# Performance work log

Measured on AMD Instinct MI355X. Metric: run time of the kernel, lower is better.

Reference implementation:

```python
import jax, jax.numpy as jnp
import numpy as np

LORA_RANK = 16
LORA_ALPHA = 32
CHUNK_SIZE = 64
TTT_LR = 0.01
SCALING = LORA_ALPHA / LORA_RANK  # 2.0

B, S = 2, 2048
K_DIM, H_DIM = 11008, 4096
EMBED_DIM, VOCAB = 4096, 32000


def setup_inputs() -> dict:
    key = jax.random.key(0)
    ks = jax.random.split(key, 7)
    x = jax.random.normal(ks[0], (B, S, K_DIM), jnp.float32) * 0.02
    input_ids = jax.random.randint(ks[1], (B, S), 0, VOCAB)
    W_base = jax.random.normal(ks[2], (H_DIM, K_DIM), jnp.float32) * 0.02
    embed_table = jax.random.normal(ks[3], (VOCAB, EMBED_DIM), jnp.float32) * 0.02
    W_proj = jax.random.normal(ks[4], (H_DIM, EMBED_DIM), jnp.float32) * 0.02
    init_A = jax.random.normal(ks[5], (H_DIM, LORA_RANK), jnp.float32) * 0.02
    init_B = jax.random.normal(ks[6], (LORA_RANK, K_DIM), jnp.float32) * 0.02
    return dict(x=x, W_base=W_base, embed_table=embed_table, W_proj=W_proj,
                init_A=init_A, init_B=init_B, input_ids=input_ids)


def reference(x, W_base, embed_table, W_proj, init_A, init_B, input_ids):
    # base (frozen) linear: x [B,S,k] @ W_base^T [k,h]
    base_out = jnp.einsum('bsk,hk->bsh', x, W_base)

    # TTT targets: embedding of NEXT token (shift-by-1, zero-padded), frozen lookup
    embeds = embed_table[input_ids]  # [B,S,E]
    shifted = jnp.concatenate([embeds[:, 1:, :], jnp.zeros_like(embeds[:, :1, :])], axis=1)
    V = jnp.einsum('bse,he->bsh', shifted, W_proj)  # [B,S,h]

    Bsz, Seq, k = x.shape
    h = W_base.shape[0]
    pad = (-Seq) % CHUNK_SIZE
    Zp = jnp.pad(x, ((0, 0), (0, pad), (0, 0)))
    Vp = jnp.pad(V, ((0, 0), (0, pad), (0, 0)))
    nc = Zp.shape[1] // CHUNK_SIZE
    Z = Zp.reshape(Bsz, nc, CHUNK_SIZE, k)    # [B,N,C,k]
    Vc = Vp.reshape(Bsz, nc, CHUNK_SIZE, h)   # [B,N,C,h]

    # per-chunk fast updates
    # dA = V^T @ (Z @ B^T) : [B,N,h,r]
    proj_in = jnp.einsum('bnck,rk->bncr', Z, init_B)
    dA = jnp.einsum('bnch,bncr->bnhr', Vc, proj_in)
    # dB = (V @ A)^T @ Z : [B,N,r,k]
    proj_err = jnp.einsum('bnch,hr->bncr', Vc, init_A)
    dB = jnp.einsum('bncr,bnck->bnrk', proj_err, Z)

    # exclusive prefix-sum over chunks (chunk i sees updates from chunks < i)
    csA = jnp.cumsum(dA, axis=1)
    csB = jnp.cumsum(dB, axis=1)
    accA = jnp.concatenate([jnp.zeros_like(csA[:, :1]), csA[:, :-1]], axis=1)
    accB = jnp.concatenate([jnp.zeros_like(csB[:, :1]), csB[:, :-1]], axis=1)

    lr = TTT_LR * SCALING
    A_eff = init_A[None, None] - lr * accA  # [B,N,h,r]
    B_eff = init_B[None, None] - lr * accB  # [B,N,r,k]

    mid = jnp.einsum('bnck,bnrk->bncr', Z, B_eff)
    lora = jnp.einsum('bncr,bnhr->bnch', mid, A_eff)  # [B,N,C,h]
    lora = lora.reshape(Bsz, nc * CHUNK_SIZE, h)[:, :Seq]
    return base_out + lora * SCALING
```

## Files before the change

kernel.cpp:

```cpp
#include <hip/hip_runtime.h>

typedef __attribute__((ext_vector_type(8))) short bf16x8;
typedef __attribute__((ext_vector_type(4))) float f32x4;

__device__ __forceinline__ float b2f(short s) {
  return __uint_as_float(((unsigned int)(unsigned short)s) << 16);
}
__device__ __forceinline__ short f2b(float f) {
  unsigned int u = __float_as_uint(f);
  unsigned int r = (u + 0x7fffu + ((u >> 16) & 1u)) >> 16;
  return (short)(unsigned short)r;
}

#define GLOAD16(g, l) __builtin_amdgcn_global_load_lds( \
    (const __attribute__((address_space(1))) void*)(g),  \
    (__attribute__((address_space(3))) void*)(l), 16, 0, 0)

__global__ __launch_bounds__(256) void prep1(const float* __restrict__ x,
    const float* __restrict__ wb, const float* __restrict__ wp,
    short* __restrict__ dst) {
  const long NX = 5636096L, NW = 11272192L, NT = 13369344L;
  for (long it = (long)blockIdx.x * 256 + threadIdx.x; it < NT;
       it += (long)gridDim.x * 256) {
    const float* s; long off;
    if (it < NX)      { s = x;  off = it; }
    else if (it < NW) { s = wb; off = it - NX; }
    else              { s = wp; off = it - NW; }
    float4 a = *(const float4*)(s + off * 8);
    float4 b = *(const float4*)(s + off * 8 + 4);
    bf16x8 o;
    o[0] = f2b(a.x); o[1] = f2b(a.y); o[2] = f2b(a.z); o[3] = f2b(a.w);
    o[4] = f2b(b.x); o[5] = f2b(b.y); o[6] = f2b(b.z); o[7] = f2b(b.w);
    *(bf16x8*)(dst + it * 8) = o;
  }
}

__global__ __launch_bounds__(256) void prep2(const float* __restrict__ initB,
    short* __restrict__ iBb, const float* __restrict__ initA,
    short* __restrict__ iAt, const float* __restrict__ emb,
    const int* __restrict__ ids, short* __restrict__ shb) {
  const long N1 = 22016L, N2 = 26112L, NT = 2123264L;
  for (long it = (long)blockIdx.x * 256 + threadIdx.x; it < NT;
       it += (long)gridDim.x * 256) {
    if (it < N1) {
      float4 a = *(const float4*)(initB + it * 8);
      float4 b = *(const float4*)(initB + it * 8 + 4);
      bf16x8 o;
      o[0] = f2b(a.x); o[1] = f2b(a.y); o[2] = f2b(a.z); o[3] = f2b(a.w);
      o[4] = f2b(b.x); o[5] = f2b(b.y); o[6] = f2b(b.z); o[7] = f2b(b.w);
      *(bf16x8*)(iBb + it * 8) = o;
    } else if (it < N2) {
      const int h = (int)(it - N1);
      #pragma unroll
      for (int r = 0; r < 16; ++r)
        iAt[(long)r * 4096 + h] = f2b(initA[(long)h * 16 + r]);
    } else {
      const long i3 = it - N2;
      const int token = (int)(i3 >> 9);
      const int e = ((int)i3 & 511) * 8;
      const int s = token & 2047;
      const int row = (s == 2047) ? -1 : ids[token + 1];
      bf16x8 o;
      if (row < 0) {
        #pragma unroll
        for (int j = 0; j < 8; ++j) o[j] = 0;
      } else {
        float4 a = *(const float4*)(emb + (long)row * 4096 + e);
        float4 b = *(const float4*)(emb + (long)row * 4096 + e + 4);
        o[0] = f2b(a.x); o[1] = f2b(a.y); o[2] = f2b(a.z); o[3] = f2b(a.w);
        o[4] = f2b(b.x); o[5] = f2b(b.y); o[6] = f2b(b.z); o[7] = f2b(b.w);
      }
      *(bf16x8*)(shb + (long)token * 4096 + e) = o;
    }
  }
}

template <int OUTBF16>
__global__ __launch_bounds__(512, 2) void gemm8p(const short* __restrict__ A,
    const short* __restrict__ B, void* __restrict__ C, int M, int N, int Kd) {
  __shared__ short lds[65536];
  const int tid = threadIdx.x;
  const int lane = tid & 63;
  const int wid = tid >> 6;
  const int wr = wid >> 2;
  const int wcn = wid & 3;
  const int l15 = lane & 15, l4 = lane >> 4, l7 = lane & 7;
  const int lb = (lane >> 3) & 1;

  const int nbx = N >> 8;
  const int cpx = gridDim.x >> 3;
  const int wg = ((int)blockIdx.x & 7) * cpx + ((int)blockIdx.x >> 3);
  const long m0 = (long)(wg / nbx) * 256;
  const long n0 = (long)(wg % nbx) * 256;

  const int NT = Kd >> 6;

  const int rho = lane >> 3;
  const short* Ag = A + (m0 + wid * 8 + rho) * (long)Kd + (l7 ^ rho) * 8;
  const short* Bg = B + (n0 + wid * 8 + rho) * (long)Kd + (l7 ^ rho) * 8;

#define STAGE_A(b, kt, c) GLOAD16(Ag + (long)(c) * 64 * Kd + (long)(kt) * 64, \
    (char*)lds + (b) * 65536 + ((c) * 8 + wid) * 1024 + lane * 16)
#define STAGE_B(b, kt, c) GLOAD16(Bg + (long)(c) * 64 * Kd + (long)(kt) * 64, \
    (char*)lds + (b) * 65536 + 32768 + ((c) * 8 + wid) * 1024 + lane * 16)

  int aLane[2];
  #pragma unroll
  for (int h = 0; h < 2; ++h)
    aLane[h] = (lb * 64 + l7 * 8 + ((h * 4 + l4) ^ l7)) * 16;

#define READ_A(dst, buf, c)                                                   \
  do {                                                                        \
    _Pragma("unroll")                                                         \
    for (int sub = 0; sub < 2; ++sub) {                                       \
      dst[sub][0] = *(const bf16x8*)((buf) + (c) * 8192 + wr * 4096 +         \
                                     sub * 2048 + aLane[0]);                  \
      dst[sub][1] = *(const bf16x8*)((buf) + (c) * 8192 + wr * 4096 +         \
                                     sub * 2048 + aLane[1]);                  \
    }                                                                         \
  } while (0)

#define READ_B(buf)                                                           \
  do {                                                                        \
    _Pragma("unroll")                                                         \
    for (int nf = 0; nf < 4; ++nf) {                                          \
      bv[nf][0] = *(const bf16x8*)((buf) + 32768 + wcn * 8192 + nf * 2048 +   \
                                   aLane[0]);                                 \
      bv[nf][1] = *(const bf16x8*)((buf) + 32768 + wcn * 8192 + nf * 2048 +   \
                                   aLane[1]);                                 \
    }                                                                         \
  } while (0)

#define MFMA_BLOCK(q, av)                                                     \
  do {                                                                        \
    _Pragma("unroll")                                                         \
    for (int sub = 0; sub < 2; ++sub)                                         \
      _Pragma("unroll")                                                       \
      for (int nf = 0; nf < 4; ++nf) {                                        \
        acc[(q) * 2 + sub][nf] = __builtin_amdgcn_mfma_f32_16x16x32_bf16(     \
            av[sub][0], bv[nf][0], acc[(q) * 2 + sub][nf], 0, 0, 0);          \
        acc[(q) * 2 + sub][nf] = __builtin_amdgcn_mfma_f32_16x16x32_bf16(     \
            av[sub][1], bv[nf][1], acc[(q) * 2 + sub][nf], 0, 0, 0);          \
      }                                                                       \
  } while (0)

  f32x4 acc[8][4];
  #pragma unroll
  for (int m = 0; m < 8; ++m)
    #pragma unroll
    for (int n = 0; n < 4; ++n) {
      acc[m][n][0] = 0.f; acc[m][n][1] = 0.f;
      acc[m][n][2] = 0.f; acc[m][n][3] = 0.f;
    }

  STAGE_A(0, 0, 0); STAGE_B(0, 0, 0);
  STAGE_A(0, 0, 1); STAGE_B(0, 0, 1);
  STAGE_A(0, 0, 2); STAGE_B(0, 0, 2);
  STAGE_A(0, 0, 3); STAGE_B(0, 0, 3);
  STAGE_A(1, 1, 0); STAGE_B(1, 1, 0);
  STAGE_A(1, 1, 1); STAGE_B(1, 1, 1);
  STAGE_A(1, 1, 2); STAGE_B(1, 1, 2);
  asm volatile("s_waitcnt vmcnt(6)" ::: "memory");
  __builtin_amdgcn_s_barrier();
  asm volatile("" ::: "memory");

  const char* ldsb = (const char*)lds;
  bf16x8 avX[2][2], avY[2][2], bv[4][2];
  READ_B(ldsb);
  READ_A(avX, ldsb, 0);

  for (int t = 0; t < NT; ++t) {
    const int cur = t & 1;
    const int tn1 = (t + 1 < NT) ? t + 1 : 0;
    const int tn2 = (t + 2 < NT) ? t + 2 : 0;
    const char* pc = ldsb + cur * 65536;
    const char* pn = ldsb + (cur ^ 1) * 65536;

    READ_A(avY, pc, 1);
    STAGE_A(cur ^ 1, tn1, 3); STAGE_B(cur ^ 1, tn1, 3);
    __builtin_amdgcn_s_barrier();
    asm volatile("s_waitcnt lgkmcnt(4)" ::: "memory");
    __builtin_amdgcn_sched_barrier(0);
    __builtin_amdgcn_s_setprio(1);
    MFMA_BLOCK(0, avX);
    __builtin_amdgcn_s_setprio(0);
    __builtin_amdgcn_s_barrier();
    asm volatile("" ::: "memory");

    READ_A(avX, pc, 2);
    STAGE_A(cur, tn2, 0); STAGE_B(cur, tn2, 0);
    __builtin_amdgcn_s_barrier();
    asm volatile("s_waitcnt lgkmcnt(4)" ::: "memory");
    __builtin_amdgcn_sched_barrier(0);
    __builtin_amdgcn_s_setprio(1);
    MFMA_BLOCK(1, avY);
    __builtin_amdgcn_s_setprio(0);
    __builtin_amdgcn_s_barrier();
    asm volatile("" ::: "memory");

    READ_A(avY, pc, 3);
    STAGE_A(cur, tn2, 1); STAGE_B(cur, tn2, 1);
    __builtin_amdgcn_s_barrier();
    asm volatile("s_waitcnt lgkmcnt(4)" ::: "memory");
    __builtin_amdgcn_sched_barrier(0);
    __builtin_amdgcn_s_setprio(1);
    MFMA_BLOCK(2, avX);
    __builtin_amdgcn_s_setprio(0);
    __builtin_amdgcn_s_barrier();
    asm volatile("" ::: "memory");

    STAGE_A(cur, tn2, 2); STAGE_B(cur, tn2, 2);
    asm volatile("s_waitcnt vmcnt(6)" ::: "memory");
    __builtin_amdgcn_s_barrier();
    asm volatile("s_waitcnt lgkmcnt(0)" ::: "memory");
    __builtin_amdgcn_sched_barrier(0);
    __builtin_amdgcn_s_setprio(1);
    MFMA_BLOCK(3, avY);
    __builtin_amdgcn_s_setprio(0);
    __builtin_amdgcn_sched_barrier(0);
    READ_B(pn);
    READ_A(avX, pn, 0);
    __builtin_amdgcn_s_barrier();
    asm volatile("" ::: "memory");
  }
#undef STAGE_A
#undef STAGE_B
#undef READ_A
#undef READ_B
#undef MFMA_BLOCK

  #pragma unroll
  for (int q = 0; q < 4; ++q)
    #pragma unroll
    for (int sub = 0; sub < 2; ++sub)
      #pragma unroll
      for (int nf = 0; nf < 4; ++nf)
        #pragma unroll
        for (int j = 0; j < 4; ++j) {
          const long row = m0 + q * 64 + wr * 32 + sub * 16 + l4 * 4 + j;
          const long col = n0 + wcn * 64 + nf * 16 + l15;
          if (OUTBF16) ((short*)C)[row * N + col] = f2b(acc[q * 2 + sub][nf][j]);
          else         ((float*)C)[row * N + col] = acc[q * 2 + sub][nf][j];
        }
}

__device__ __forceinline__ void gemv_core(short* lds, const short* __restrict__ A,
    const short* __restrict__ W, float* __restrict__ part, int Kd, int Klen,
    long wStride) {
  const int tid = threadIdx.x;
  const int lane = tid & 63;
  const int w = tid >> 6;
  const int l15 = lane & 15, l4 = lane >> 4;
  const int rho = lane >> 3, j7 = lane & 7;
  const long m0 = (long)blockIdx.x * 64;
  const long k0 = (long)blockIdx.y * Klen;
  const int NTk = Klen >> 6;
  const short* Wr = W + (wStride ? (long)blockIdx.x * wStride : 0);
  const short* Ag = A + (m0 + w * 8 + rho) * (long)Kd + k0 + (j7 ^ rho) * 8;

#define STG(b, kt, i) GLOAD16(Ag + (long)(i) * 32 * Kd + (long)(kt) * 64, \
    (char*)lds + (b) * 8192 + ((i) * 4 + w) * 1024 + lane * 16)

  int aOff[2];
  #pragma unroll
  for (int kk = 0; kk < 2; ++kk)
    aOff[kk] = ((w * 16 + l15) >> 3) * 1024 + (l15 & 7) * 128 +
               (((kk * 4 + l4) ^ (l15 & 7)) * 16);

  f32x4 acc; acc[0] = 0.f; acc[1] = 0.f; acc[2] = 0.f; acc[3] = 0.f;

  STG(0, 0, 0); STG(0, 0, 1);
  for (int t = 0; t < NTk; ++t) {
    const int cur = t & 1;
    const int tn = (t + 1 < NTk) ? t + 1 : 0;
    const short* wp = Wr + (long)l15 * Kd + k0 + (long)t * 64 + l4 * 8;
    bf16x8 wv0 = *(const bf16x8*)(wp);
    bf16x8 wv1 = *(const bf16x8*)(wp + 32);
    STG(cur ^ 1, tn, 0); STG(cur ^ 1, tn, 1);
    asm volatile("s_waitcnt vmcnt(2)" ::: "memory");
    __builtin_amdgcn_s_barrier();
    bf16x8 a0 = *(const bf16x8*)((const char*)lds + cur * 8192 + aOff[0]);
    bf16x8 a1 = *(const bf16x8*)((const char*)lds + cur * 8192 + aOff[1]);
    asm volatile("s_waitcnt lgkmcnt(0)" ::: "memory");
    __builtin_amdgcn_sched_barrier(0);
    acc = __builtin_amdgcn_mfma_f32_16x16x32_bf16(a0, wv0, acc, 0, 0, 0);
    acc = __builtin_amdgcn_mfma_f32_16x16x32_bf16(a1, wv1, acc, 0, 0, 0);
    __builtin_amdgcn_s_barrier();
  }
#undef STG

  float* dst = part + (long)blockIdx.y * 65536;
  #pragma unroll
  for (int r = 0; r < 4; ++r)
    dst[(m0 + w * 16 + l4 * 4 + r) * 16 + l15] = acc[r];
}

__global__ __launch_bounds__(256) void gemv_pinper(const short* __restrict__ xb,
    const short* __restrict__ iBb, float* __restrict__ pinP,
    const short* __restrict__ Vb, const short* __restrict__ iAt,
    float* __restrict__ perP) {
  __shared__ short lds[8192];
  if (blockIdx.z == 0) gemv_core(lds, xb, iBb, pinP, 11008, 2752, 0L);
  else                 gemv_core(lds, Vb, iAt, perP, 4096, 1024, 0L);
}

__global__ __launch_bounds__(256) void gemv_mid(const short* __restrict__ xb,
    const short* __restrict__ Beff, float* __restrict__ midP) {
  __shared__ short lds[8192];
  gemv_core(lds, xb, Beff, midP, 11008, 2752, 176128L);
}

__global__ __launch_bounds__(256) void dAdB_kernel(const short* __restrict__ V,
    const short* __restrict__ X, const float* __restrict__ pinP,
    const float* __restrict__ perP, float* __restrict__ dA,
    float* __restrict__ dB) {
  const int chunk = blockIdx.y;
  __shared__ float ps[1024];
  if (blockIdx.x < 16) {
    const int h = blockIdx.x * 256 + threadIdx.x;
    #pragma unroll
    for (int i = 0; i < 4; ++i) {
      const long o = (long)chunk * 1024 + i * 256 + threadIdx.x;
      ps[i * 256 + threadIdx.x] = pinP[o] + pinP[o + 65536] +
                                  pinP[o + 131072] + pinP[o + 196608];
    }
    __syncthreads();
    float acc[16];
    #pragma unroll
    for (int r = 0; r < 16; ++r) acc[r] = 0.f;
    for (int c = 0; c < 64; ++c) {
      const float v = b2f(V[((long)chunk * 64 + c) * 4096 + h]);
      #pragma unroll
      for (int r = 0; r < 16; ++r) acc[r] = fmaf(v, ps[c * 16 + r], acc[r]);
    }
    float* dst = dA + ((long)chunk * 4096 + h) * 16;
    #pragma unroll
    for (int i = 0; i < 4; ++i) {
      f32x4 w; w[0] = acc[i*4]; w[1] = acc[i*4+1]; w[2] = acc[i*4+2]; w[3] = acc[i*4+3];
      *(f32x4*)(dst + i * 4) = w;
    }
  } else {
    const int k = (blockIdx.x - 16) * 256 + threadIdx.x;
    #pragma unroll
    for (int i = 0; i < 4; ++i) {
      const long o = (long)chunk * 1024 + i * 256 + threadIdx.x;
      ps[i * 256 + threadIdx.x] = perP[o] + perP[o + 65536] +
                                  perP[o + 131072] + perP[o + 196608];
    }
    __syncthreads();
    float acc[16];
    #pragma unroll
    for (int r = 0; r < 16; ++r) acc[r] = 0.f;
    for (int c = 0; c < 64; ++c) {
      const float xv = b2f(X[((long)chunk * 64 + c) * 11008 + k]);
      #pragma unroll
      for (int r = 0; r < 16; ++r) acc[r] = fmaf(xv, ps[c * 16 + r], acc[r]);
    }
    #pragma unroll
    for (int r = 0; r < 16; ++r)
      dB[((long)chunk * 16 + r) * 11008 + k] = acc[r];
  }
}

__global__ __launch_bounds__(256) void scan_kernel(const float* __restrict__ dA,
    const float* __restrict__ initA, short* __restrict__ Aeff,
    const float* __restrict__ dB, const float* __restrict__ initB,
    short* __restrict__ Beff) {
  const int b = blockIdx.y;
  if (blockIdx.x < 256) {
    const long idx = (long)blockIdx.x * 256 + threadIdx.x;
    const float a0 = initA[idx];
    float acc = 0.f;
    for (int n = 0; n < 32; ++n) {
      const long chunk = (long)b * 32 + n;
      Aeff[chunk * 65536 + idx] = f2b(a0 - 0.02f * acc);
      acc += dA[chunk * 65536 + idx];
    }
  } else {
    const long idx = (long)(blockIdx.x - 256) * 256 + threadIdx.x;
    const float b0 = initB[idx];
    float acc = 0.f;
    for (int n = 0; n < 32; ++n) {
      const long chunk = (long)b * 32 + n;
      Beff[chunk * 176128 + idx] = f2b(b0 - 0.02f * acc);
      acc += dB[chunk * 176128 + idx];
    }
  }
}

__global__ __launch_bounds__(256) void final_kernel(const short* __restrict__ base,
    const float* __restrict__ midP, const short* __restrict__ Aeff,
    float* __restrict__ out) {
  const int token = blockIdx.x;
  const int chunk = token >> 6;
  __shared__ float m[16];
  if (threadIdx.x < 16) {
    const long o = (long)token * 16 + threadIdx.x;
    m[threadIdx.x] = midP[o] + midP[o + 65536] + midP[o + 131072] + midP[o + 196608];
  }
  __syncthreads();
  float mf[16];
  #pragma unroll
  for (int r = 0; r < 16; ++r) mf[r] = m[r];
  for (int it = 0; it < 2; ++it) {
    const int h0 = it * 2048 + threadIdx.x * 8;
    bf16x8 bs = *(const bf16x8*)(base + (long)token * 4096 + h0);
    float res[8];
    #pragma unroll
    for (int j = 0; j < 8; ++j) {
      const short* ar = Aeff + ((long)chunk * 4096 + h0 + j) * 16;
      bf16x8 a0 = *(const bf16x8*)ar;
      bf16x8 a1 = *(const bf16x8*)(ar + 8);
      float s = 0.f;
      #pragma unroll
      for (int r = 0; r < 8; ++r) {
        s = fmaf(mf[r], b2f(a0[r]), s);
        s = fmaf(mf[r + 8], b2f(a1[r]), s);
      }
      res[j] = b2f(bs[j]) + 2.0f * s;
    }
    #pragma unroll
    for (int i = 0; i < 2; ++i) {
      f32x4 w; w[0] = res[i*4]; w[1] = res[i*4+1]; w[2] = res[i*4+2]; w[3] = res[i*4+3];
      *(f32x4*)(out + (long)token * 4096 + h0 + i * 4) = w;
    }
  }
}

extern "C" void kernel_launch(void* const* d_in, const int* in_sizes, int n_in,
                              void* d_out, int out_size, void* d_ws, size_t ws_size,
                              hipStream_t stream) {
  const float* x     = (const float*)d_in[0];
  const float* Wbase = (const float*)d_in[1];
  const float* emb   = (const float*)d_in[2];
  const float* Wproj = (const float*)d_in[3];
  const float* initA = (const float*)d_in[4];
  const float* initB = (const float*)d_in[5];
  const int*   ids   = (const int*)d_in[6];
  float* outp = (float*)d_out;

  char* p = (char*)d_ws;
  short* xb   = (short*)p; p += 90177536L;
  short* Wb   = (short*)p; p += 90177536L;
  short* Wpb  = (short*)p; p += 33554432L;
  short* shb  = (short*)p; p += 33554432L;
  short* Vb   = (short*)p; p += 33554432L;
  short* base = (short*)p; p += 33554432L;
  short* iBb  = (short*)p; p += 352256L;
  short* iAt  = (short*)p; p += 131072L;
  short* Aeff = (short*)p; p += 8388608L;
  short* Beff = (short*)p; p += 22544384L;
  float* pinP = (float*)p; p += 1048576L;
  float* perP = (float*)p; p += 1048576L;
  float* midP = (float*)p; p += 1048576L;
  float* dA = (float*)Wpb;
  float* dB = (float*)((char*)Wpb + 16777216L);

  prep1<<<2048, 256, 0, stream>>>(x, Wbase, Wproj, xb);
  prep2<<<2048, 256, 0, stream>>>(initB, iBb, initA, iAt, emb, ids, shb);

  gemm8p<1><<<256, 512, 0, stream>>>(shb, Wpb, (void*)Vb, 4096, 4096, 4096);
  gemm8p<1><<<256, 512, 0, stream>>>(xb, Wb, (void*)base, 4096, 4096, 11008);

  gemv_pinper<<<dim3(64, 4, 2), 256, 0, stream>>>(xb, iBb, pinP, Vb, iAt, perP);
  dAdB_kernel<<<dim3(59, 64), 256, 0, stream>>>(Vb, xb, pinP, perP, dA, dB);
  scan_kernel<<<dim3(944, 2), 256, 0, stream>>>(dA, initA, Aeff, dB, initB, Beff);

  gemv_mid<<<dim3(64, 4), 256, 0, stream>>>(xb, Beff, midP);
  final_kernel<<<4096, 256, 0, stream>>>(base, midP, Aeff, outp);
}
```

Before: 732.0 us.

## Fuse LoRA epilogue into base GEMM and drop final kernel

The base GEMM moves to the end of the pipeline and gains an epilogue. It reduces the midP partials into LDS, computes the rank-16 LoRA correction from Aeff, and writes fp32 output directly. This removes the bf16 base intermediate (its write and later read) and the separate final kernel launch. The GEMM epilogue gets heavier and can no longer overlap with the scan and gemv stages, and the base result now stays in fp32 rather than being rounded to bf16.

```diff
diff --git a/kernel.cpp b/kernel.cpp
--- a/kernel.cpp
+++ b/kernel.cpp
@@ -75,9 +75,11 @@
   }
 }
 
-template <int OUTBF16>
+template <int FUSE>
 __global__ __launch_bounds__(512, 2) void gemm8p(const short* __restrict__ A,
-    const short* __restrict__ B, void* __restrict__ C, int M, int N, int Kd) {
+    const short* __restrict__ B, void* __restrict__ C,
+    const float* __restrict__ midP, const short* __restrict__ Aeff,
+    int M, int N, int Kd) {
   __shared__ short lds[65536];
   const int tid = threadIdx.x;
   const int lane = tid & 63;
@@ -229,19 +231,78 @@
 #undef READ_B
 #undef MFMA_BLOCK
 
-  #pragma unroll
-  for (int q = 0; q < 4; ++q)
-    #pragma unroll
-    for (int sub = 0; sub < 2; ++sub)
-      #pragma unroll
-      for (int nf = 0; nf < 4; ++nf)
+  if (FUSE) {
+    asm volatile("s_waitcnt vmcnt(0) lgkmcnt(0)" ::: "memory");
+    __builtin_amdgcn_s_barrier();
+    float* mlds = (float*)lds;
+    {
+      const long o0 = m0 * 16 + tid * 8;
+      #pragma unroll
+      for (int half = 0; half < 2; ++half) {
+        f32x4 v;
+        v[0] = 0.f; v[1] = 0.f; v[2] = 0.f; v[3] = 0.f;
+        #pragma unroll
+        for (int s = 0; s < 4; ++s) {
+          f32x4 tv = *(const f32x4*)(midP + o0 + half * 4 + (long)s * 65536);
+          v[0] += tv[0]; v[1] += tv[1]; v[2] += tv[2]; v[3] += tv[3];
+        }
+        *(f32x4*)(mlds + tid * 8 + half * 4) = v;
+      }
+    }
+    __builtin_amdgcn_s_barrier();
+    const long chunk0 = m0 >> 6;
+    float* out = (float*)C;
+    #pragma unroll
+    for (int q = 0; q < 4; ++q) {
+      float af[4][16];
+      #pragma unroll
+      for (int nf = 0; nf < 4; ++nf) {
+        const long col = n0 + wcn * 64 + nf * 16 + l15;
+        const short* ap = Aeff + ((chunk0 + q) * 4096 + col) * 16;
+        bf16x8 a0 = *(const bf16x8*)ap;
+        bf16x8 a1 = *(const bf16x8*)(ap + 8);
+        #pragma unroll
+        for (int r = 0; r < 8; ++r) {
+          af[nf][r] = b2f(a0[r]);
+          af[nf][r + 8] = b2f(a1[r]);
+        }
+      }
+      #pragma unroll
+      for (int sub = 0; sub < 2; ++sub)
         #pragma unroll
         for (int j = 0; j < 4; ++j) {
-          const long row = m0 + q * 64 + wr * 32 + sub * 16 + l4 * 4 + j;
-          const long col = n0 + wcn * 64 + nf * 16 + l15;
-          if (OUTBF16) ((short*)C)[row * N + col] = f2b(acc[q * 2 + sub][nf][j]);
-          else         ((float*)C)[row * N + col] = acc[q * 2 + sub][nf][j];
+          const int rl = q * 64 + wr * 32 + sub * 16 + l4 * 4 + j;
+          float mf[16];
+          #pragma unroll
+          for (int hh = 0; hh < 4; ++hh) {
+            f32x4 mv = *(const f32x4*)(mlds + rl * 16 + hh * 4);
+            mf[hh * 4] = mv[0]; mf[hh * 4 + 1] = mv[1];
+            mf[hh * 4 + 2] = mv[2]; mf[hh * 4 + 3] = mv[3];
+          }
+          #pragma unroll
+          for (int nf = 0; nf < 4; ++nf) {
+            float s = 0.f;
+            #pragma unroll
+            for (int r = 0; r < 16; ++r) s = fmaf(mf[r], af[nf][r], s);
+            const long col = n0 + wcn * 64 + nf * 16 + l15;
+            out[(m0 + rl) * N + col] = acc[q * 2 + sub][nf][j] + 2.0f * s;
+          }
         }
+    }
+  } else {
+    #pragma unroll
+    for (int q = 0; q < 4; ++q)
+      #pragma unroll
+      for (int sub = 0; sub < 2; ++sub)
+        #pragma unroll
+        for (int nf = 0; nf < 4; ++nf)
+          #pragma unroll
+          for (int j = 0; j < 4; ++j) {
+            const long row = m0 + q * 64 + wr * 32 + sub * 16 + l4 * 4 + j;
+            const long col = n0 + wcn * 64 + nf * 16 + l15;
+            ((short*)C)[row * N + col] = f2b(acc[q * 2 + sub][nf][j]);
+          }
+  }
 }
 
 __device__ __forceinline__ void gemv_core(short* lds, const short* __restrict__ A,
@@ -388,45 +449,6 @@
   }
 }
 
-__global__ __launch_bounds__(256) void final_kernel(const short* __restrict__ base,
-    const float* __restrict__ midP, const short* __restrict__ Aeff,
-    float* __restrict__ out) {
-  const int token = blockIdx.x;
-  const int chunk = token >> 6;
-  __shared__ float m[16];
-  if (threadIdx.x < 16) {
-    const long o = (long)token * 16 + threadIdx.x;
-    m[threadIdx.x] = midP[o] + midP[o + 65536] + midP[o + 131072] + midP[o + 196608];
-  }
-  __syncthreads();
-  float mf[16];
-  #pragma unroll
-  for (int r = 0; r < 16; ++r) mf[r] = m[r];
-  for (int it = 0; it < 2; ++it) {
-    const int h0 = it * 2048 + threadIdx.x * 8;
-    bf16x8 bs = *(const bf16x8*)(base + (long)token * 4096 + h0);
-    float res[8];
-    #pragma unroll
-    for (int j = 0; j < 8; ++j) {
-      const short* ar = Aeff + ((long)chunk * 4096 + h0 + j) * 16;
-      bf16x8 a0 = *(const bf16x8*)ar;
-      bf16x8 a1 = *(const bf16x8*)(ar + 8);
-      float s = 0.f;
-      #pragma unroll
-      for (int r = 0; r < 8; ++r) {
-        s = fmaf(mf[r], b2f(a0[r]), s);
-        s = fmaf(mf[r + 8], b2f(a1[r]), s);
-      }
-      res[j] = b2f(bs[j]) + 2.0f * s;
-    }
-    #pragma unroll
-    for (int i = 0; i < 2; ++i) {
-      f32x4 w; w[0] = res[i*4]; w[1] = res[i*4+1]; w[2] = res[i*4+2]; w[3] = res[i*4+3];
-      *(f32x4*)(out + (long)token * 4096 + h0 + i * 4) = w;
-    }
-  }
-}
-
 extern "C" void kernel_launch(void* const* d_in, const int* in_sizes, int n_in,
                               void* d_out, int out_size, void* d_ws, size_t ws_size,
                               hipStream_t stream) {
@@ -445,7 +467,6 @@
   short* Wpb  = (short*)p; p += 33554432L;
   short* shb  = (short*)p; p += 33554432L;
   short* Vb   = (short*)p; p += 33554432L;
-  short* base = (short*)p; p += 33554432L;
   short* iBb  = (short*)p; p += 352256L;
   short* iAt  = (short*)p; p += 131072L;
   short* Aeff = (short*)p; p += 8388608L;
@@ -459,13 +480,14 @@
   prep1<<<2048, 256, 0, stream>>>(x, Wbase, Wproj, xb);
   prep2<<<2048, 256, 0, stream>>>(initB, iBb, initA, iAt, emb, ids, shb);
 
-  gemm8p<1><<<256, 512, 0, stream>>>(shb, Wpb, (void*)Vb, 4096, 4096, 4096);
-  gemm8p<1><<<256, 512, 0, stream>>>(xb, Wb, (void*)base, 4096, 4096, 11008);
+  gemm8p<0><<<256, 512, 0, stream>>>(shb, Wpb, (void*)Vb, nullptr, nullptr,
+                                     4096, 4096, 4096);
 
   gemv_pinper<<<dim3(64, 4, 2), 256, 0, stream>>>(xb, iBb, pinP, Vb, iAt, perP);
   dAdB_kernel<<<dim3(59, 64), 256, 0, stream>>>(Vb, xb, pinP, perP, dA, dB);
   scan_kernel<<<dim3(944, 2), 256, 0, stream>>>(dA, initA, Aeff, dB, initB, Beff);
-
   gemv_mid<<<dim3(64, 4), 256, 0, stream>>>(xb, Beff, midP);
-  final_kernel<<<4096, 256, 0, stream>>>(base, midP, Aeff, outp);
-}
+
+  gemm8p<1><<<256, 512, 0, stream>>>(xb, Wb, (void*)outp, midP, Aeff,
+                                     4096, 4096, 11008);
+}
```

Result: faster. 669.5 us (-8.5%).
